# Kernel optimization log

Measured on AMD Instinct MI355X. Metric: run time of the kernel, lower is better.

## Reference

```python
import jax, jax.numpy as jnp
import numpy as np
from jax import lax

EMB, HID, L, PATCH, IMG, K = 192, 64, 6, 4, 224, 8
FMAP = IMG // PATCH
N = FMAP * FMAP
B = 8
ALG = 4
GB_np = np.array([0, 1, 1, 2])  # grade of each blade [1, e1, e2, e12]
GB = jnp.asarray(GB_np)

def _cayley_np():
    C = np.zeros((4, 4, 4), np.float32)
    tbl = {(0,0):(0,1.),(0,1):(1,1.),(0,2):(2,1.),(0,3):(3,1.),
           (1,0):(1,1.),(1,1):(0,1.),(1,2):(3,1.),(1,3):(2,1.),
           (2,0):(2,1.),(2,1):(3,-1.),(2,2):(0,1.),(2,3):(1,-1.),
           (3,0):(3,1.),(3,1):(2,-1.),(3,2):(1,1.),(3,3):(0,-1.)}
    for (i, j), (k, s) in tbl.items():
        C[i, j, k] = s
    return C

CAY_np = _cayley_np()
CAYLEY = jnp.asarray(CAY_np)
_paths = np.zeros((3, 3, 3), bool)
for _i in range(4):
    for _j in range(4):
        for _k in range(4):
            if CAY_np[_i, _j, _k] != 0:
                _paths[GB_np[_i], GB_np[_j], GB_np[_k]] = True
PI, PJ, PK = (jnp.asarray(a) for a in np.nonzero(_paths))
NPATH = int(_paths.sum())  # 10 geometric-product paths for Cl(2,0)

def build_knn_graph(H, W, k):
    yy, xx = np.meshgrid(np.arange(H, dtype=np.float32), np.arange(W, dtype=np.float32), indexing='ij')
    coords = np.stack([xx.ravel(), yy.ravel()], -1)
    cn = coords / np.array([W - 1, H - 1], np.float32) * 2 - 1
    d = np.linalg.norm(cn[:, None] - cn[None], axis=-1)
    np.fill_diagonal(d, np.inf)
    idx = np.argsort(d, axis=-1, kind='stable')[:, :k]
    rows = np.repeat(np.arange(H * W), k)
    cols = idx.reshape(-1)
    return rows.astype(np.int32), cols.astype(np.int32), cn.astype(np.float32)

def mvlin(x, W, b=None):
    # per-grade MVLinear: W [out,in,3] expanded to blades via GB
    y = jnp.einsum('nmi,bmi->bni', W[:, :, GB], x)
    if b is not None:
        y = y.at[:, :, 0].add(b)  # bias embedded in scalar blade only
    return y

def mvlin_flat(x, W, b):
    # subspaces=False MVLinear: same weight across blades
    y = jnp.einsum('nm,bmi->bni', W, x)
    return y.at[:, :, 0].add(b)

def mv_silu(x, a, b):
    # invariants: [scalar, q(grade1), q(grade2)]; gate = sigmoid(a*inv+b)
    inv = jnp.concatenate([x[..., :1], x[..., 1:2]**2 + x[..., 2:3]**2, x[..., 3:4]**2], -1)
    return jax.nn.sigmoid(a * inv + b)[..., GB] * x

def normalize_mv(x, a):
    q = jnp.concatenate([x[..., :1]**2, x[..., 1:2]**2 + x[..., 2:3]**2, x[..., 3:4]**2], -1)
    n = jnp.sqrt(q + 1e-12)
    d = jax.nn.sigmoid(a) * (n - 1.0) + 1.0
    return x / (d + 1e-6)[..., GB]

def sgp(x, Wl, bl, Wr, na, gw):
    # SteerableGeometricProductLayer
    xr = normalize_mv(mvlin(x, Wr), na)
    full = jnp.zeros((gw.shape[0], 3, 3, 3), x.dtype).at[:, PI, PJ, PK].set(gw)
    fb = full[:, GB][:, :, GB][:, :, :, GB]  # [feat,4,4,4]
    gp = jnp.einsum('bni,nijk,bnk->bnj', x, CAYLEY[None] * fb, xr)
    return (mvlin(x, Wl, bl) + gp) * np.float32(1.0 / np.sqrt(2.0))

def _forward(x, conv_w, conv_b, stem_g, stem_b, pos_embed, in_W, in_b, in_Wl, in_bl, in_Wr, in_na, in_gw, eg_eW, eg_eb, eg_sa, eg_sb, eg_nW, eg_nb, eg_Wl, eg_bl, eg_Wr, eg_na, eg_gw, eg_aa, eg_ab, out_W, out_b, on_g, on_b, cls_W, cls_b, coords, rows, cols):
    Bx = x.shape[0]
    # stem: strided conv + LayerNorm over (C,H,W)
    y = lax.conv_general_dilated(x, conv_w, (PATCH, PATCH), 'VALID', dimension_numbers=('NCHW', 'OIHW', 'NCHW')) + conv_b[None, :, None, None]
    mu = y.mean(axis=(1, 2, 3), keepdims=True)
    var = ((y - mu) ** 2).mean(axis=(1, 2, 3), keepdims=True)
    y = (y - mu) / jnp.sqrt(var + 1e-5) * stem_g[None] + stem_b[None]
    y = y + pos_embed
    feat = y.transpose(0, 2, 3, 1).reshape(Bx * N, EMB)
    # embed features in scalar blade, coordinates in vector blades e1,e2
    h = jnp.zeros((Bx * N, EMB + 1, ALG), x.dtype)
    h = h.at[:, :EMB, 0].set(feat)
    h = h.at[:, EMB, 1:3].set(jnp.tile(coords, (Bx, 1)))
    h = sgp(mvlin_flat(h, in_W, in_b), in_Wl, in_bl, in_Wr, in_na, in_gw)
    BN = Bx * N
    for i in range(L):
        m = mv_silu(mvlin(h[rows] - h[cols], eg_eW[i], eg_eb[i]), eg_sa[i], eg_sb[i])
        agg = jax.ops.segment_sum(m, rows, num_segments=BN)  # count computed but unused in original
        nu = mvlin(jnp.concatenate([h, agg], axis=1), eg_nW[i], eg_nb[i])
        out = mv_silu(sgp(nu, eg_Wl[i], eg_bl[i], eg_Wr[i], eg_na[i], eg_gw[i]), eg_aa[i], eg_ab[i])
        h = h + out if i > 0 else out
    s = mvlin_flat(h, out_W, out_b)[..., 0]
    mu2 = s.mean(-1, keepdims=True)
    v2 = ((s - mu2) ** 2).mean(-1, keepdims=True)
    s = (s - mu2) / jnp.sqrt(v2 + 1e-5) * on_g + on_b
    pooled = s.reshape(Bx, N, EMB).mean(axis=1)
    return pooled @ cls_W.T + cls_b

def setup_inputs() -> dict:
    key = jax.random.key(0)
    ks = iter(jax.random.split(key, 64))
    nrm = lambda shape, s=0.05: jax.random.normal(next(ks), shape, jnp.float32) * s
    rows, cols, cn = build_knn_graph(FMAP, FMAP, K)
    offs = np.arange(B, dtype=np.int32)[:, None] * N
    rows_b = (rows[None] + offs).reshape(-1)
    cols_b = (cols[None] + offs).reshape(-1)
    return dict(
        x=jax.random.normal(next(ks), (B, 3, IMG, IMG), jnp.float32),
        conv_w=nrm((EMB, 3, PATCH, PATCH)),
        conv_b=jnp.zeros((EMB,), jnp.float32),
        stem_g=jnp.ones((EMB, FMAP, FMAP), jnp.float32),
        stem_b=jnp.zeros((EMB, FMAP, FMAP), jnp.float32),
        pos_embed=nrm((1, EMB, FMAP, FMAP), 0.02),
        coords=jnp.asarray(cn),
        in_W=nrm((HID, EMB + 1)), in_b=jnp.zeros((HID,), jnp.float32),
        in_Wl=nrm((HID, HID, 3)), in_bl=jnp.zeros((HID,), jnp.float32),
        in_Wr=nrm((HID, HID, 3)), in_na=jnp.zeros((HID, 3), jnp.float32),
        in_gw=nrm((HID, NPATH), 0.2),
        eg_eW=nrm((L, HID, HID, 3)), eg_eb=jnp.zeros((L, HID), jnp.float32),
        eg_sa=jnp.ones((L, HID, 3), jnp.float32), eg_sb=jnp.zeros((L, HID, 3), jnp.float32),
        eg_nW=nrm((L, HID, 2 * HID, 3)), eg_nb=jnp.zeros((L, HID), jnp.float32),
        eg_Wl=nrm((L, HID, HID, 3)), eg_bl=jnp.zeros((L, HID), jnp.float32),
        eg_Wr=nrm((L, HID, HID, 3)), eg_na=jnp.zeros((L, HID, 3), jnp.float32),
        eg_gw=nrm((L, HID, NPATH), 0.2),
        eg_aa=jnp.ones((L, HID, 3), jnp.float32), eg_ab=jnp.zeros((L, HID, 3), jnp.float32),
        out_W=nrm((EMB, HID)), out_b=jnp.zeros((EMB,), jnp.float32),
        on_g=jnp.ones((EMB,), jnp.float32), on_b=jnp.zeros((EMB,), jnp.float32),
        cls_W=nrm((10, EMB), 0.02), cls_b=jnp.zeros((10,), jnp.float32),
        rows=jnp.asarray(rows_b), cols=jnp.asarray(cols_b),
    )

def reference(x, conv_w, conv_b, stem_g, stem_b, pos_embed, coords, in_W, in_b, in_Wl, in_bl, in_Wr, in_na, in_gw, eg_eW, eg_eb, eg_sa, eg_sb, eg_nW, eg_nb, eg_Wl, eg_bl, eg_Wr, eg_na, eg_gw, eg_aa, eg_ab, out_W, out_b, on_g, on_b, cls_W, cls_b, rows, cols):
    return _forward(x, conv_w, conv_b, stem_g, stem_b, pos_embed, in_W, in_b, in_Wl, in_bl, in_Wr, in_na, in_gw, eg_eW, eg_eb, eg_sa, eg_sb, eg_nW, eg_nb, eg_Wl, eg_bl, eg_Wr, eg_na, eg_gw, eg_aa, eg_ab, out_W, out_b, on_g, on_b, cls_W, cls_b, coords, rows, cols)
```

## Files before the change

kernel.cpp:

```cpp
#include <hip/hip_runtime.h>
#include <hip/hip_bf16.h>
#include <math.h>

#define EMBC   192
#define NLAY   6
#define IMGC   224
#define FMAPC  56
#define NNODE  3136
#define NBATCH 8
#define BNODES 25088
#define KNNE   8
#define NT     32
#define RSQRT2 0.70710678118654752f

__device__ __forceinline__ float sigm(float x){ return 1.0f/(1.0f+__expf(-x)); }

__global__ void k_repackw(const float* __restrict__ src, float* __restrict__ dst, int K){
  int l = blockIdx.y;
  size_t S = (size_t)64*K*3;
  int t = blockIdx.x*256 + threadIdx.x;
  if(t < (int)S){
    int j = t % 3; int r = t / 3;
    int cw = r % 16; int m = (r / 16) % K; int widx = r / (16*K);
    dst[l*S + (((size_t)widx*K + m)*16 + cw)*3 + j] =
      src[l*S + ((size_t)(widx*16+cw)*K + m)*3 + j];
  }
}
__global__ void k_repack1(const float* __restrict__ src, float* __restrict__ dst,
                          int R, int K){
  int t = blockIdx.x*256 + threadIdx.x;
  if(t < R*K){
    int m = t % K, r = t / K;
    dst[m*R + r] = src[r*K + m];
  }
}

__global__ void k_tr(const float* __restrict__ g, const float* __restrict__ sb,
                     const float* __restrict__ pe, float* __restrict__ g2,
                     float* __restrict__ pb2){
  int n = blockIdx.x; int c = threadIdx.x;
  g2[n*EMBC + c]  = g[c*NNODE + n];
  pb2[n*EMBC + c] = sb[c*NNODE + n] + pe[c*NNODE + n];
}

__global__ __launch_bounds__(256) void k_conv(const float* __restrict__ x,
    const float* __restrict__ cw, const float* __restrict__ cb,
    float* __restrict__ y0, float* __restrict__ parts){
  __shared__ float xs[2688];
  __shared__ float wsh[9216];
  __shared__ float red[512];
  int blk = blockIdx.x; int b = blk / FMAPC; int ph = blk % FMAPC;
  int tid = threadIdx.x;
  for(int t = tid; t < 9216; t += 256) wsh[t] = cw[t];
  for(int t = tid; t < 2688; t += 256){
    int r = t / IMGC; int w = t % IMGC;
    int ci = r >> 2, kh = r & 3;
    xs[t] = x[((size_t)(b*3 + ci)*IMGC + (ph*4 + kh))*IMGC + w];
  }
  __syncthreads();
  float s1 = 0.f, s2 = 0.f;
  for(int oi = tid; oi < FMAPC*EMBC; oi += 256){
    int pw = oi / EMBC; int c = oi % EMBC;
    float acc = cb[c];
    const float4* wv4 = (const float4*)(wsh + c*48);
    #pragma unroll
    for(int r = 0; r < 12; ++r){
      float4 xv = *((const float4*)(xs + r*IMGC + pw*4));
      float4 wv = wv4[r];
      acc += xv.x*wv.x + xv.y*wv.y + xv.z*wv.z + xv.w*wv.w;
    }
    y0[((size_t)(b*NNODE + ph*FMAPC + pw))*EMBC + c] = acc;
    s1 += acc; s2 += acc*acc;
  }
  red[tid] = s1; red[256+tid] = s2;
  __syncthreads();
  for(int st = 128; st > 0; st >>= 1){
    if(tid < st){ red[tid] += red[tid+st]; red[256+tid] += red[256+tid+st]; }
    __syncthreads();
  }
  if(tid == 0){ parts[blk*2] = red[0]; parts[blk*2+1] = red[256]; }
}

__global__ void k_stats(const float* __restrict__ parts, float* __restrict__ stats){
  int b = threadIdx.x;
  if(b < NBATCH){
    float S = 0.f, Q = 0.f;
    for(int j = 0; j < FMAPC; ++j){ S += parts[(b*FMAPC+j)*2]; Q += parts[(b*FMAPC+j)*2+1]; }
    float cnt = (float)(EMBC*NNODE);
    float mu = S/cnt;
    float var = Q/cnt - mu*mu;
    stats[b*2] = mu; stats[b*2+1] = rsqrtf(var + 1e-5f);
  }
}

__global__ __launch_bounds__(256,2) void k_embed(const float* __restrict__ y0,
    const float* __restrict__ stats, const float* __restrict__ g2,
    const float* __restrict__ pb2, const float* __restrict__ inWp,
    const float* __restrict__ inb, const float* __restrict__ coords,
    float* __restrict__ xmv){
  __shared__ float fs[64*193];
  int tid = threadIdx.x, lane = tid & 63;
  int wid = __builtin_amdgcn_readfirstlane(tid >> 6);
  int ch0 = wid << 4;
  int bid = blockIdx.x;
  int blk = (bid & 7)*49 + (bid >> 3);
  int p0 = blk * 64;
  int b = p0 / NNODE; int n0 = p0 - b*NNODE;
  float mu = stats[b*2], rstd = stats[b*2+1];
  for(int t = tid; t < 64*192; t += 256){
    int n = t / 192, c = t - n*192;
    int nn = n0 + n;
    fs[n*193 + c] = (y0[(size_t)(p0+n)*192 + c] - mu)*rstd*g2[nn*192+c] + pb2[nn*192+c];
  }
  __syncthreads();
  float acc[16];
  #pragma unroll
  for(int ci = 0; ci < 16; ++ci) acc[ci] = 0.f;
  #pragma unroll 2
  for(int m = 0; m < 192; ++m){
    float xm = fs[lane*193 + m];
    const float* wp = inWp + m*64 + ch0;
    #pragma unroll
    for(int ci = 0; ci < 16; ++ci) acc[ci] += wp[ci]*xm;
  }
  float cx = coords[(n0+lane)*2], cy = coords[(n0+lane)*2+1];
  #pragma unroll
  for(int ci = 0; ci < 16; ++ci){
    int ch = ch0 + ci;
    float wc = inWp[192*64 + ch];
    float4 v; v.x = acc[ci] + inb[ch]; v.y = wc*cx; v.z = wc*cy; v.w = 0.f;
    *((float4*)(xmv + ((size_t)(p0+lane)*64 + ch)*4)) = v;
  }
}

__device__ __forceinline__ void stage_x(float* xs, const float* __restrict__ g,
                                        int p0, int tid){
  #pragma unroll
  for(int t = tid; t < NT*64; t += 256){
    int n = t >> 6, m = t & 63;
    *((float4*)(xs + (n<<8) + (((m + n)&63)<<2))) =
      *((const float4*)(g + (((size_t)(p0+n))<<8) + (m<<2)));
  }
}
__device__ __forceinline__ void copyout(const float* xs, float* __restrict__ g,
                                        int p0, int tid){
  #pragma unroll
  for(int t = tid; t < NT*64; t += 256){
    int n = t >> 6, m = t & 63;
    float4 v = *((const float4*)(xs + (n<<8) + (((m + n)&63)<<2)));
    *((float4*)(g + (((size_t)(p0+n))<<8) + (m<<2))) = v;
  }
}
__device__ __forceinline__ void stage_w(float* wst, const float* __restrict__ Wp,
                                        int K, int moff, int tid){
  #pragma unroll
  for(int t = tid; t < 3072; t += 256){
    int c = t / 768, r = t - c*768;
    ((float4*)wst)[t] = ((const float4*)(Wp + ((size_t)(c*K + moff)*48)))[r];
  }
}
__device__ __forceinline__ void mm2n(float (&pA)[4][4], float (&pB)[4][4],
    const float* __restrict__ wst, const float* __restrict__ xrA,
    const float* __restrict__ xrB, int wb, int np){
  #pragma unroll 4
  for(int m = 0; m < 64; ++m){
    float4 xa = *((const float4*)(xrA + (((m + np)&63)<<2)));
    float4 xb = *((const float4*)(xrB + (((m + np + 16)&63)<<2)));
    const float* wp = wst + wb + m*48;
    float4 a = *((const float4*)wp);
    float4 b = *((const float4*)(wp+4));
    float4 c = *((const float4*)(wp+8));
    pA[0][0]+=a.x*xa.x; pA[0][1]+=a.y*xa.y; pA[0][2]+=a.y*xa.z; pA[0][3]+=a.z*xa.w;
    pA[1][0]+=a.w*xa.x; pA[1][1]+=b.x*xa.y; pA[1][2]+=b.x*xa.z; pA[1][3]+=b.y*xa.w;
    pA[2][0]+=b.z*xa.x; pA[2][1]+=b.w*xa.y; pA[2][2]+=b.w*xa.z; pA[2][3]+=c.x*xa.w;
    pA[3][0]+=c.y*xa.x; pA[3][1]+=c.z*xa.y; pA[3][2]+=c.z*xa.z; pA[3][3]+=c.w*xa.w;
    pB[0][0]+=a.x*xb.x; pB[0][1]+=a.y*xb.y; pB[0][2]+=a.y*xb.z; pB[0][3]+=a.z*xb.w;
    pB[1][0]+=a.w*xb.x; pB[1][1]+=b.x*xb.y; pB[1][2]+=b.x*xb.z; pB[1][3]+=b.y*xb.w;
    pB[2][0]+=b.z*xb.x; pB[2][1]+=b.w*xb.y; pB[2][2]+=b.w*xb.z; pB[2][3]+=c.x*xb.w;
    pB[3][0]+=c.y*xb.x; pB[3][1]+=c.z*xb.y; pB[3][2]+=c.z*xb.z; pB[3][3]+=c.w*xb.w;
  }
}
#define ZERO44(A) { _Pragma("unroll") for(int _i=0;_i<4;++_i) _Pragma("unroll") for(int _j=0;_j<4;++_j) A[_i][_j]=0.f; }

__global__ __launch_bounds__(256,2) void k_sgp0(const float* __restrict__ src,
    float* __restrict__ h, float* __restrict__ zout,
    const float* __restrict__ Wlp, const float* __restrict__ bl,
    const float* __restrict__ Wrp, const float* __restrict__ na,
    const float* __restrict__ gw, const float* __restrict__ zWp){
  __shared__ float xs[NT*256];
  __shared__ float wst[12288];
  int tid = threadIdx.x, lane = tid & 63;
  int widx = __builtin_amdgcn_readfirstlane(tid >> 6);
  int np = lane & 15, qw = lane >> 4;
  int ch0 = widx*16 + qw*4;
  int wb = widx*3072 + qw*12;
  int bid = blockIdx.x;
  int blk = (bid & 7)*98 + (bid >> 3);
  int p0 = blk * NT;
  const float* xrA = xs + (np<<8);
  const float* xrB = xs + ((np+16)<<8);
  stage_x(xs, src, p0, tid);
  stage_w(wst, Wlp, 64, 0, tid);
  __syncthreads();
  float lA[4][4], lB[4][4];
  ZERO44(lA); ZERO44(lB);
  mm2n(lA, lB, wst, xrA, xrB, wb, np);
  __syncthreads();
  stage_w(wst, Wrp, 64, 0, tid);
  __syncthreads();
  float rA[4][4], rB[4][4];
  ZERO44(rA); ZERO44(rB);
  mm2n(rA, rB, wst, xrA, xrB, wb, np);
  float oA[4][4], oB[4][4];
  #pragma unroll
  for(int j = 0; j < 2; ++j){
    int nn = np + j*16;
    #pragma unroll
    for(int ci = 0; ci < 4; ++ci){
      int ch = ch0 + ci;
      float yr0 = j? rB[ci][0]:rA[ci][0], yr1 = j? rB[ci][1]:rA[ci][1];
      float yr2 = j? rB[ci][2]:rA[ci][2], yr3 = j? rB[ci][3]:rA[ci][3];
      float na0 = sigm(na[ch*3]), na1 = sigm(na[ch*3+1]), na2 = sigm(na[ch*3+2]);
      float d0 = na0*(sqrtf(yr0*yr0 + 1e-12f) - 1.f) + 1.f + 1e-6f;
      float d1 = na1*(sqrtf(yr1*yr1 + yr2*yr2 + 1e-12f) - 1.f) + 1.f + 1e-6f;
      float d2 = na2*(sqrtf(yr3*yr3 + 1e-12f) - 1.f) + 1.f + 1e-6f;
      float xq0 = yr0/d0, xq1 = yr1/d1, xq2 = yr2/d1, xq3 = yr3/d2;
      float4 xv = *((const float4*)(xs + (nn<<8) + (((ch + nn)&63)<<2)));
      const float* gwp = gw + ch*10;
      float gp0 = gwp[0]*xv.x*xq0 + gwp[3]*(xv.y*xq1 + xv.z*xq2) + gwp[7]*xv.w*xq3;
      float gp1 = gwp[1]*xv.x*xq1 + gwp[4]*xv.y*xq0 - gwp[5]*xv.z*xq3 - gwp[8]*xv.w*xq2;
      float gp2 = gwp[1]*xv.x*xq2 + gwp[4]*xv.z*xq0 + gwp[5]*xv.y*xq3 + gwp[8]*xv.w*xq1;
      float gp3 = gwp[2]*xv.x*xq3 + gwp[6]*(xv.y*xq2 - xv.z*xq1) - gwp[9]*xv.w*xq0;
      float l0 = j? lB[ci][0]:lA[ci][0], l1 = j? lB[ci][1]:lA[ci][1];
      float l2 = j? lB[ci][2]:lA[ci][2], l3 = j? lB[ci][3]:lA[ci][3];
      float* o = j? oB[ci] : oA[ci];
      o[0] = (l0 + bl[ch] + gp0)*RSQRT2;
      o[1] = (l1 + gp1)*RSQRT2;
      o[2] = (l2 + gp2)*RSQRT2;
      o[3] = (l3 + gp3)*RSQRT2;
    }
  }
  __syncthreads();
  #pragma unroll
  for(int ci = 0; ci < 4; ++ci){
    int ch = ch0 + ci;
    float4 v0; v0.x=oA[ci][0]; v0.y=oA[ci][1]; v0.z=oA[ci][2]; v0.w=oA[ci][3];
    *((float4*)(xs + (np<<8) + (((ch + np)&63)<<2))) = v0;
    float4 v1; v1.x=oB[ci][0]; v1.y=oB[ci][1]; v1.z=oB[ci][2]; v1.w=oB[ci][3];
    *((float4*)(xs + ((np+16)<<8) + (((ch + np + 16)&63)<<2))) = v1;
  }
  __syncthreads();
  copyout(xs, h, p0, tid);
  stage_w(wst, zWp, 64, 0, tid);
  __syncthreads();
  float zA[4][4], zB[4][4];
  ZERO44(zA); ZERO44(zB);
  mm2n(zA, zB, wst, xrA, xrB, wb, np);
  __syncthreads();
  #pragma unroll
  for(int ci = 0; ci < 4; ++ci){
    int ch = ch0 + ci;
    float4 v0; v0.x=zA[ci][0]; v0.y=zA[ci][1]; v0.z=zA[ci][2]; v0.w=zA[ci][3];
    *((float4*)(xs + (np<<8) + (((ch + np)&63)<<2))) = v0;
    float4 v1; v1.x=zB[ci][0]; v1.y=zB[ci][1]; v1.z=zB[ci][2]; v1.w=zB[ci][3];
    *((float4*)(xs + ((np+16)<<8) + (((ch + np + 16)&63)<<2))) = v1;
  }
  __syncthreads();
  copyout(xs, zout, p0, tid);
}

__global__ __launch_bounds__(256,2) void k_layer(
    float* __restrict__ h, const float* __restrict__ z,
    float* __restrict__ zout, const int* __restrict__ cols,
    const float* __restrict__ eb, const float* __restrict__ sa,
    const float* __restrict__ sb,
    const float* __restrict__ nWp, const float* __restrict__ nb,
    const float* __restrict__ Wlp, const float* __restrict__ bl,
    const float* __restrict__ Wrp, const float* __restrict__ na,
    const float* __restrict__ gw, const float* __restrict__ aa,
    const float* __restrict__ ab,
    const float* __restrict__ zWp, int mode){
  __shared__ float xs[NT*256];
  __shared__ float wst[12288];
  int tid = threadIdx.x, lane = tid & 63;
  int widx = __builtin_amdgcn_readfirstlane(tid >> 6);
  int np = lane & 15, qw = lane >> 4;
  int ch0 = widx*16 + qw*4;
  int wb = widx*3072 + qw*12;
  int bid = blockIdx.x;
  int blk = (bid & 7)*98 + (bid >> 3);
  int p0 = blk * NT;
  const float* xrA = xs + (np<<8);
  const float* xrB = xs + ((np+16)<<8);
  float ag[8][4];
  {
    int ch = lane;
    float ebv = eb[ch];
    float a0 = sa[ch*3], a1 = sa[ch*3+1], a2 = sa[ch*3+2];
    float b0 = sb[ch*3], b1 = sb[ch*3+1], b2 = sb[ch*3+2];
    #pragma unroll
    for(int e = 0; e < 8; ++e){
      int p = p0 + widx*8 + e;
      float4 zo = *((const float4*)(z + ((size_t)p*64 + ch)*4));
      float ax=0.f, ay=0.f, az_=0.f, aw=0.f;
      #pragma unroll
      for(int k = 0; k < KNNE; ++k){
        int c = cols[p*KNNE + k];
        float4 zc = *((const float4*)(z + ((size_t)c*64 + ch)*4));
        float d0 = zo.x - zc.x + ebv;
        float d1 = zo.y - zc.y;
        float d2 = zo.z - zc.z;
        float d3 = zo.w - zc.w;
        float g0 = sigm(a0*d0 + b0);
        float g1 = sigm(a1*(d1*d1 + d2*d2) + b1);
        float g2v = sigm(a2*(d3*d3) + b2);
        ax += g0*d0; ay += g1*d1; az_ += g1*d2; aw += g2v*d3;
      }
      ag[e][0]=ax; ag[e][1]=ay; ag[e][2]=az_; ag[e][3]=aw;
    }
  }
  stage_x(xs, h, p0, tid);
  stage_w(wst, nWp, 128, 0, tid);
  __syncthreads();
  float nuA[4][4], nuB[4][4];
  ZERO44(nuA); ZERO44(nuB);
  mm2n(nuA, nuB, wst, xrA, xrB, wb, np);
  float hrA[4][4], hrB[4][4];
  if(mode == 2){
    #pragma unroll
    for(int ci = 0; ci < 4; ++ci){
      int ch = ch0 + ci;
      float4 v0 = *((const float4*)(xrA + (((ch + np)&63)<<2)));
      float4 v1 = *((const float4*)(xrB + (((ch + np + 16)&63)<<2)));
      hrA[ci][0]=v0.x; hrA[ci][1]=v0.y; hrA[ci][2]=v0.z; hrA[ci][3]=v0.w;
      hrB[ci][0]=v1.x; hrB[ci][1]=v1.y; hrB[ci][2]=v1.z; hrB[ci][3]=v1.w;
    }
  }
  __syncthreads();
  #pragma unroll
  for(int e = 0; e < 8; ++e){
    int nn = widx*8 + e;
    float4 v; v.x=ag[e][0]; v.y=ag[e][1]; v.z=ag[e][2]; v.w=ag[e][3];
    *((float4*)(xs + (nn<<8) + (((lane + nn)&63)<<2))) = v;
  }
  stage_w(wst, nWp, 128, 64, tid);
  __syncthreads();
  mm2n(nuA, nuB, wst, xrA, xrB, wb, np);
  __syncthreads();
  #pragma unroll
  for(int ci = 0; ci < 4; ++ci){
    int ch = ch0 + ci;
    nuA[ci][0] += nb[ch]; nuB[ci][0] += nb[ch];
    float4 v0; v0.x=nuA[ci][0]; v0.y=nuA[ci][1]; v0.z=nuA[ci][2]; v0.w=nuA[ci][3];
    *((float4*)(xs + (np<<8) + (((ch + np)&63)<<2))) = v0;
    float4 v1; v1.x=nuB[ci][0]; v1.y=nuB[ci][1]; v1.z=nuB[ci][2]; v1.w=nuB[ci][3];
    *((float4*)(xs + ((np+16)<<8) + (((ch + np + 16)&63)<<2))) = v1;
  }
  stage_w(wst, Wlp, 64, 0, tid);
  __syncthreads();
  float lA[4][4], lB[4][4];
  ZERO44(lA); ZERO44(lB);
  mm2n(lA, lB, wst, xrA, xrB, wb, np);
  __syncthreads();
  stage_w(wst, Wrp, 64, 0, tid);
  __syncthreads();
  float rA[4][4], rB[4][4];
  ZERO44(rA); ZERO44(rB);
  mm2n(rA, rB, wst, xrA, xrB, wb, np);
  float oA[4][4], oB[4][4];
  #pragma unroll
  for(int j = 0; j < 2; ++j){
    #pragma unroll
    for(int ci = 0; ci < 4; ++ci){
      int ch = ch0 + ci;
      float yr0 = j? rB[ci][0]:rA[ci][0], yr1 = j? rB[ci][1]:rA[ci][1];
      float yr2 = j? rB[ci][2]:rA[ci][2], yr3 = j? rB[ci][3]:rA[ci][3];
      float na0 = sigm(na[ch*3]), na1 = sigm(na[ch*3+1]), na2 = sigm(na[ch*3+2]);
      float d0 = na0*(sqrtf(yr0*yr0 + 1e-12f) - 1.f) + 1.f + 1e-6f;
      float d1 = na1*(sqrtf(yr1*yr1 + yr2*yr2 + 1e-12f) - 1.f) + 1.f + 1e-6f;
      float d2 = na2*(sqrtf(yr3*yr3 + 1e-12f) - 1.f) + 1.f + 1e-6f;
      float xq0 = yr0/d0, xq1 = yr1/d1, xq2 = yr2/d1, xq3 = yr3/d2;
      float x0 = j? nuB[ci][0]:nuA[ci][0], x1 = j? nuB[ci][1]:nuA[ci][1];
      float x2 = j? nuB[ci][2]:nuA[ci][2], x3 = j? nuB[ci][3]:nuA[ci][3];
      const float* gwp = gw + ch*10;
      float gp0 = gwp[0]*x0*xq0 + gwp[3]*(x1*xq1 + x2*xq2) + gwp[7]*x3*xq3;
      float gp1 = gwp[1]*x0*xq1 + gwp[4]*x1*xq0 - gwp[5]*x2*xq3 - gwp[8]*x3*xq2;
      float gp2 = gwp[1]*x0*xq2 + gwp[4]*x2*xq0 + gwp[5]*x1*xq3 + gwp[8]*x3*xq1;
      float gp3 = gwp[2]*x0*xq3 + gwp[6]*(x1*xq2 - x2*xq1) - gwp[9]*x3*xq0;
      float l0 = j? lB[ci][0]:lA[ci][0], l1 = j? lB[ci][1]:lA[ci][1];
      float l2 = j? lB[ci][2]:lA[ci][2], l3 = j? lB[ci][3]:lA[ci][3];
      float o0 = (l0 + bl[ch] + gp0)*RSQRT2;
      float o1 = (l1 + gp1)*RSQRT2;
      float o2 = (l2 + gp2)*RSQRT2;
      float o3 = (l3 + gp3)*RSQRT2;
      float g0 = sigm(aa[ch*3]*o0 + ab[ch*3]);
      float g1 = sigm(aa[ch*3+1]*(o1*o1 + o2*o2) + ab[ch*3+1]);
      float g2v = sigm(aa[ch*3+2]*(o3*o3) + ab[ch*3+2]);
      float v0 = g0*o0, v1 = g1*o1, v2 = g1*o2, v3 = g2v*o3;
      if(mode == 2){
        if(j){ v0 += hrB[ci][0]; v1 += hrB[ci][1]; v2 += hrB[ci][2]; v3 += hrB[ci][3]; }
        else { v0 += hrA[ci][0]; v1 += hrA[ci][1]; v2 += hrA[ci][2]; v3 += hrA[ci][3]; }
      }
      float* o = j? oB[ci] : oA[ci];
      o[0]=v0; o[1]=v1; o[2]=v2; o[3]=v3;
    }
  }
  __syncthreads();
  #pragma unroll
  for(int ci = 0; ci < 4; ++ci){
    int ch = ch0 + ci;
    float4 v0; v0.x=oA[ci][0]; v0.y=oA[ci][1]; v0.z=oA[ci][2]; v0.w=oA[ci][3];
    *((float4*)(xs + (np<<8) + (((ch + np)&63)<<2))) = v0;
    float4 v1; v1.x=oB[ci][0]; v1.y=oB[ci][1]; v1.z=oB[ci][2]; v1.w=oB[ci][3];
    *((float4*)(xs + ((np+16)<<8) + (((ch + np + 16)&63)<<2))) = v1;
  }
  __syncthreads();
  copyout(xs, h, p0, tid);
  if(zWp != nullptr){
    stage_w(wst, zWp, 64, 0, tid);
    __syncthreads();
    float zA[4][4], zB[4][4];
    ZERO44(zA); ZERO44(zB);
    mm2n(zA, zB, wst, xrA, xrB, wb, np);
    __syncthreads();
    #pragma unroll
    for(int ci = 0; ci < 4; ++ci){
      int ch = ch0 + ci;
      float4 v0; v0.x=zA[ci][0]; v0.y=zA[ci][1]; v0.z=zA[ci][2]; v0.w=zA[ci][3];
      *((float4*)(xs + (np<<8) + (((ch + np)&63)<<2))) = v0;
      float4 v1; v1.x=zB[ci][0]; v1.y=zB[ci][1]; v1.z=zB[ci][2]; v1.w=zB[ci][3];
      *((float4*)(xs + ((np+16)<<8) + (((ch + np + 16)&63)<<2))) = v1;
    }
    __syncthreads();
    copyout(xs, zout, p0, tid);
  }
}

__global__ __launch_bounds__(256,2) void k_head(const float* __restrict__ h,
    const float* __restrict__ oWp, const float* __restrict__ ob,
    const float* __restrict__ ong, const float* __restrict__ onb,
    float* __restrict__ s){
  __shared__ float hs[64*65];
  __shared__ float rr[512];
  int tid = threadIdx.x, lane = tid & 63;
  int wid = __builtin_amdgcn_readfirstlane(tid >> 6);
  int c0 = wid*48;
  int bid = blockIdx.x;
  int blk = (bid & 7)*49 + (bid >> 3);
  int p0 = blk * 64;
  for(int t = tid; t < 64*64; t += 256){
    int nn = t >> 6, c = t & 63;
    hs[nn*65 + c] = h[(((size_t)(p0+nn))*64 + c)*4];
  }
  __syncthreads();
  float a[48];
  #pragma unroll
  for(int ci = 0; ci < 48; ++ci) a[ci] = 0.f;
  #pragma unroll 2
  for(int m = 0; m < 64; ++m){
    float xm = hs[lane*65 + m];
    const float* wp = oWp + m*192 + c0;
    #pragma unroll
    for(int ci = 0; ci < 48; ++ci) a[ci] += wp[ci]*xm;
  }
  float s1 = 0.f, s2 = 0.f;
  #pragma unroll
  for(int ci = 0; ci < 48; ++ci){
    a[ci] += ob[c0+ci];
    s1 += a[ci]; s2 += a[ci]*a[ci];
  }
  rr[wid*64 + lane] = s1; rr[256 + wid*64 + lane] = s2;
  __syncthreads();
  float S = rr[lane] + rr[64+lane] + rr[128+lane] + rr[192+lane];
  float Q = rr[256+lane] + rr[320+lane] + rr[384+lane] + rr[448+lane];
  float mu = S*(1.0f/EMBC);
  float var = Q*(1.0f/EMBC) - mu*mu;
  float rstd = rsqrtf(var + 1e-5f);
  #pragma unroll
  for(int q = 0; q < 12; ++q){
    int c = c0 + q*4;
    float4 v;
    v.x = (a[q*4  ] - mu)*rstd*ong[c  ] + onb[c  ];
    v.y = (a[q*4+1] - mu)*rstd*ong[c+1] + onb[c+1];
    v.z = (a[q*4+2] - mu)*rstd*ong[c+2] + onb[c+2];
    v.w = (a[q*4+3] - mu)*rstd*ong[c+3] + onb[c+3];
    *((float4*)(s + (size_t)(p0+lane)*192 + c)) = v;
  }
}

__global__ void k_pool1(const float* __restrict__ s, float* __restrict__ pp){
  int blk = blockIdx.x;
  int b = blk >> 5, chunk = blk & 31;
  int c = threadIdx.x;
  float acc = 0.f;
  int n0 = chunk*98;
  for(int j = 0; j < 98; ++j) acc += s[((size_t)(b*NNODE + n0 + j))*EMBC + c];
  pp[(size_t)blk*EMBC + c] = acc;
}
__global__ void k_pool2(const float* __restrict__ pp, float* __restrict__ pooled){
  int b = blockIdx.x; int c = threadIdx.x;
  float acc = 0.f;
  for(int j = 0; j < 32; ++j) acc += pp[((size_t)(b*32 + j))*EMBC + c];
  pooled[b*EMBC + c] = acc * (1.0f/NNODE);
}

__global__ void k_cls(const float* __restrict__ pooled, const float* __restrict__ cW,
                      const float* __restrict__ cb, float* __restrict__ out){
  int tid = threadIdx.x;
  if(tid < NBATCH*10){
    int b = tid/10, k = tid%10;
    float acc = cb[k];
    for(int c = 0; c < EMBC; ++c) acc += pooled[b*EMBC + c]*cW[k*EMBC + c];
    out[tid] = acc;
  }
}

extern "C" void kernel_launch(void* const* d_in, const int* in_sizes, int n_in,
                              void* d_out, int out_size, void* d_ws, size_t ws_size,
                              hipStream_t stream){
  const float* x      = (const float*)d_in[0];
  const float* conv_w = (const float*)d_in[1];
  const float* conv_b = (const float*)d_in[2];
  const float* stem_g = (const float*)d_in[3];
  const float* stem_b = (const float*)d_in[4];
  const float* pos_e  = (const float*)d_in[5];
  const float* coords = (const float*)d_in[6];
  const float* inW    = (const float*)d_in[7];
  const float* inb    = (const float*)d_in[8];
  const float* inWl   = (const float*)d_in[9];
  const float* inbl   = (const float*)d_in[10];
  const float* inWr   = (const float*)d_in[11];
  const float* inna   = (const float*)d_in[12];
  const float* ingw   = (const float*)d_in[13];
  const float* eg_eW  = (const float*)d_in[14];
  const float* eg_eb  = (const float*)d_in[15];
  const float* eg_sa  = (const float*)d_in[16];
  const float* eg_sb  = (const float*)d_in[17];
  const float* eg_nW  = (const float*)d_in[18];
  const float* eg_nb  = (const float*)d_in[19];
  const float* eg_Wl  = (const float*)d_in[20];
  const float* eg_bl  = (const float*)d_in[21];
  const float* eg_Wr  = (const float*)d_in[22];
  const float* eg_na  = (const float*)d_in[23];
  const float* eg_gw  = (const float*)d_in[24];
  const float* eg_aa  = (const float*)d_in[25];
  const float* eg_ab  = (const float*)d_in[26];
  const float* outW   = (const float*)d_in[27];
  const float* outb   = (const float*)d_in[28];
  const float* ong    = (const float*)d_in[29];
  const float* onb    = (const float*)d_in[30];
  const float* clsW   = (const float*)d_in[31];
  const float* clsb   = (const float*)d_in[32];
  const int*   cols   = (const int*)d_in[34];

  float* ws = (float*)d_ws;
  size_t off = 0;
  float* hbuf  = ws + off; off += (size_t)BNODES*256;
  float* bigA  = ws + off; off += (size_t)BNODES*256;
  float* bigB  = ws + off; off += (size_t)BNODES*256;
  float* g2    = ws + off; off += (size_t)NNODE*EMBC;
  float* pb2   = ws + off; off += (size_t)NNODE*EMBC;
  float* parts = ws + off; off += 896;
  float* stats = ws + off; off += 16;
  float* pp    = ws + off; off += 256*EMBC;
  float* pooled= ws + off; off += NBATCH*EMBC;
  float* wpInW = ws + off; off += 193*64;
  float* wpOW  = ws + off; off += 64*192;
  float* wpInWl= ws + off; off += 12288;
  float* wpInWr= ws + off; off += 12288;
  float* wpEW  = ws + off; off += (size_t)NLAY*12288;
  float* wpWl  = ws + off; off += (size_t)NLAY*12288;
  float* wpWr  = ws + off; off += (size_t)NLAY*12288;
  float* wpNW  = ws + off; off += (size_t)NLAY*24576;
  float* y0    = bigB;

  const int NTILE = BNODES/NT;

  { dim3 g1((12352+255)/256); k_repack1<<<g1, 256, 0, stream>>>(inW,  wpInW, 64, 193); }
  { dim3 g1((12288+255)/256); k_repack1<<<g1, 256, 0, stream>>>(outW, wpOW, 192, 64); }
  { dim3 g3((12288+255)/256, 1); k_repackw<<<g3, 256, 0, stream>>>(inWl, wpInWl, 64); }
  { dim3 g3((12288+255)/256, 1); k_repackw<<<g3, 256, 0, stream>>>(inWr, wpInWr, 64); }
  { dim3 g3((12288+255)/256, NLAY); k_repackw<<<g3, 256, 0, stream>>>(eg_eW, wpEW, 64); }
  { dim3 g3((12288+255)/256, NLAY); k_repackw<<<g3, 256, 0, stream>>>(eg_Wl, wpWl, 64); }
  { dim3 g3((12288+255)/256, NLAY); k_repackw<<<g3, 256, 0, stream>>>(eg_Wr, wpWr, 64); }
  { dim3 g3((24576+255)/256, NLAY); k_repackw<<<g3, 256, 0, stream>>>(eg_nW, wpNW, 128); }

  k_tr   <<<NNODE, 192, 0, stream>>>(stem_g, stem_b, pos_e, g2, pb2);
  k_conv <<<NBATCH*FMAPC, 256, 0, stream>>>(x, conv_w, conv_b, y0, parts);
  k_stats<<<1, 64, 0, stream>>>(parts, stats);
  k_embed<<<BNODES/64, 256, 0, stream>>>(y0, stats, g2, pb2, wpInW, inb, coords, bigA);
  k_sgp0 <<<NTILE, 256, 0, stream>>>(bigA, hbuf, bigB, wpInWl, inbl, wpInWr,
                                     inna, ingw, wpEW);
  float* zcur = bigB;
  float* spare = bigA;
  for(int l = 0; l < NLAY; ++l){
    const float* zWn = (l < NLAY-1) ? (wpEW + (size_t)(l+1)*12288) : (const float*)nullptr;
    k_layer<<<NTILE, 256, 0, stream>>>(hbuf, zcur, spare, cols,
        eg_eb + l*64, eg_sa + l*192, eg_sb + l*192,
        wpNW + (size_t)l*24576, eg_nb + l*64,
        wpWl + (size_t)l*12288, eg_bl + l*64,
        wpWr + (size_t)l*12288, eg_na + l*192,
        eg_gw + l*640, eg_aa + l*192, eg_ab + l*192,
        zWn, (l==0)?1:2);
    if(l < NLAY-1){ float* t = zcur; zcur = spare; spare = t; }
  }
  k_head <<<BNODES/64, 256, 0, stream>>>(hbuf, wpOW, outb, ong, onb, spare);
  k_pool1<<<256, 192, 0, stream>>>(spare, pp);
  k_pool2<<<8, 192, 0, stream>>>(pp, pooled);
  k_cls  <<<1, 128, 0, stream>>>(pooled, clsW, clsb, (float*)d_out);
}
```

Baseline: 1.493 ms.

## Stream weights in 16-row chunks to shrink LDS and raise occupancy

Weight staging is split into four 16-input-channel chunks per matmul, each staged between barriers, so the LDS weight buffer shrinks from 48KB to 12KB. Launch bounds rise from 2 to 3 blocks per CU to use the freed LDS for more resident workgroups. The cost is four times as many barriers and smaller, unoverlapped global-to-LDS loads per pass, plus tighter register limits that may cause spilling.

```diff
diff --git a/kernel.cpp b/kernel.cpp
--- a/kernel.cpp
+++ b/kernel.cpp
@@ -151,21 +151,22 @@
     *((float4*)(g + (((size_t)(p0+n))<<8) + (m<<2))) = v;
   }
 }
-__device__ __forceinline__ void stage_w(float* wst, const float* __restrict__ Wp,
-                                        int K, int moff, int tid){
-  #pragma unroll
-  for(int t = tid; t < 3072; t += 256){
-    int c = t / 768, r = t - c*768;
+__device__ __forceinline__ void stage_w16(float* wst, const float* __restrict__ Wp,
+                                          int K, int moff, int tid){
+  #pragma unroll
+  for(int t = tid; t < 768; t += 256){
+    int c = t / 192, r = t - c*192;
     ((float4*)wst)[t] = ((const float4*)(Wp + ((size_t)(c*K + moff)*48)))[r];
   }
 }
-__device__ __forceinline__ void mm2n(float (&pA)[4][4], float (&pB)[4][4],
+__device__ __forceinline__ void mm2n16(float (&pA)[4][4], float (&pB)[4][4],
     const float* __restrict__ wst, const float* __restrict__ xrA,
-    const float* __restrict__ xrB, int wb, int np){
+    const float* __restrict__ xrB, int wb, int np, int mo){
   #pragma unroll 4
-  for(int m = 0; m < 64; ++m){
-    float4 xa = *((const float4*)(xrA + (((m + np)&63)<<2)));
-    float4 xb = *((const float4*)(xrB + (((m + np + 16)&63)<<2)));
+  for(int m = 0; m < 16; ++m){
+    int mg = mo + m;
+    float4 xa = *((const float4*)(xrA + (((mg + np)&63)<<2)));
+    float4 xb = *((const float4*)(xrB + (((mg + np + 16)&63)<<2)));
     const float* wp = wst + wb + m*48;
     float4 a = *((const float4*)wp);
     float4 b = *((const float4*)(wp+4));
@@ -180,37 +181,44 @@
     pB[3][0]+=c.y*xb.x; pB[3][1]+=c.z*xb.y; pB[3][2]+=c.z*xb.z; pB[3][3]+=c.w*xb.w;
   }
 }
+__device__ __forceinline__ void mmpass(float (&pA)[4][4], float (&pB)[4][4],
+    float* wst, const float* __restrict__ Wp, int K, int mbase,
+    const float* __restrict__ xrA, const float* __restrict__ xrB,
+    int wb, int np, int tid){
+  #pragma unroll
+  for(int mo = 0; mo < 64; mo += 16){
+    __syncthreads();
+    stage_w16(wst, Wp, K, mbase + mo, tid);
+    __syncthreads();
+    mm2n16(pA, pB, wst, xrA, xrB, wb, np, mo);
+  }
+}
 #define ZERO44(A) { _Pragma("unroll") for(int _i=0;_i<4;++_i) _Pragma("unroll") for(int _j=0;_j<4;++_j) A[_i][_j]=0.f; }
 
-__global__ __launch_bounds__(256,2) void k_sgp0(const float* __restrict__ src,
+__global__ __launch_bounds__(256,3) void k_sgp0(const float* __restrict__ src,
     float* __restrict__ h, float* __restrict__ zout,
     const float* __restrict__ Wlp, const float* __restrict__ bl,
     const float* __restrict__ Wrp, const float* __restrict__ na,
     const float* __restrict__ gw, const float* __restrict__ zWp){
   __shared__ float xs[NT*256];
-  __shared__ float wst[12288];
+  __shared__ float wst[3072];
   int tid = threadIdx.x, lane = tid & 63;
   int widx = __builtin_amdgcn_readfirstlane(tid >> 6);
   int np = lane & 15, qw = lane >> 4;
   int ch0 = widx*16 + qw*4;
-  int wb = widx*3072 + qw*12;
+  int wb = widx*768 + qw*12;
   int bid = blockIdx.x;
   int blk = (bid & 7)*98 + (bid >> 3);
   int p0 = blk * NT;
   const float* xrA = xs + (np<<8);
   const float* xrB = xs + ((np+16)<<8);
   stage_x(xs, src, p0, tid);
-  stage_w(wst, Wlp, 64, 0, tid);
-  __syncthreads();
   float lA[4][4], lB[4][4];
   ZERO44(lA); ZERO44(lB);
-  mm2n(lA, lB, wst, xrA, xrB, wb, np);
-  __syncthreads();
-  stage_w(wst, Wrp, 64, 0, tid);
-  __syncthreads();
+  mmpass(lA, lB, wst, Wlp, 64, 0, xrA, xrB, wb, np, tid);
   float rA[4][4], rB[4][4];
   ZERO44(rA); ZERO44(rB);
-  mm2n(rA, rB, wst, xrA, xrB, wb, np);
+  mmpass(rA, rB, wst, Wrp, 64, 0, xrA, xrB, wb, np, tid);
   float oA[4][4], oB[4][4];
   #pragma unroll
   for(int j = 0; j < 2; ++j){
@@ -251,11 +259,9 @@
   }
   __syncthreads();
   copyout(xs, h, p0, tid);
-  stage_w(wst, zWp, 64, 0, tid);
-  __syncthreads();
   float zA[4][4], zB[4][4];
   ZERO44(zA); ZERO44(zB);
-  mm2n(zA, zB, wst, xrA, xrB, wb, np);
+  mmpass(zA, zB, wst, zWp, 64, 0, xrA, xrB, wb, np, tid);
   __syncthreads();
   #pragma unroll
   for(int ci = 0; ci < 4; ++ci){
@@ -269,7 +275,7 @@
   copyout(xs, zout, p0, tid);
 }
 
-__global__ __launch_bounds__(256,2) void k_layer(
+__global__ __launch_bounds__(256,3) void k_layer(
     float* __restrict__ h, const float* __restrict__ z,
     float* __restrict__ zout, const int* __restrict__ cols,
     const float* __restrict__ eb, const float* __restrict__ sa,
@@ -281,12 +287,12 @@
     const float* __restrict__ ab,
     const float* __restrict__ zWp, int mode){
   __shared__ float xs[NT*256];
-  __shared__ float wst[12288];
+  __shared__ float wst[3072];
   int tid = threadIdx.x, lane = tid & 63;
   int widx = __builtin_amdgcn_readfirstlane(tid >> 6);
   int np = lane & 15, qw = lane >> 4;
   int ch0 = widx*16 + qw*4;
-  int wb = widx*3072 + qw*12;
+  int wb = widx*768 + qw*12;
   int bid = blockIdx.x;
   int blk = (bid & 7)*98 + (bid >> 3);
   int p0 = blk * NT;
@@ -320,11 +326,9 @@
     }
   }
   stage_x(xs, h, p0, tid);
-  stage_w(wst, nWp, 128, 0, tid);
-  __syncthreads();
   float nuA[4][4], nuB[4][4];
   ZERO44(nuA); ZERO44(nuB);
-  mm2n(nuA, nuB, wst, xrA, xrB, wb, np);
+  mmpass(nuA, nuB, wst, nWp, 128, 0, xrA, xrB, wb, np, tid);
   float hrA[4][4], hrB[4][4];
   if(mode == 2){
     #pragma unroll
@@ -343,9 +347,7 @@
     float4 v; v.x=ag[e][0]; v.y=ag[e][1]; v.z=ag[e][2]; v.w=ag[e][3];
     *((float4*)(xs + (nn<<8) + (((lane + nn)&63)<<2))) = v;
   }
-  stage_w(wst, nWp, 128, 64, tid);
-  __syncthreads();
-  mm2n(nuA, nuB, wst, xrA, xrB, wb, np);
+  mmpass(nuA, nuB, wst, nWp, 128, 64, xrA, xrB, wb, np, tid);
   __syncthreads();
   #pragma unroll
   for(int ci = 0; ci < 4; ++ci){
@@ -356,17 +358,12 @@
     float4 v1; v1.x=nuB[ci][0]; v1.y=nuB[ci][1]; v1.z=nuB[ci][2]; v1.w=nuB[ci][3];
     *((float4*)(xs + ((np+16)<<8) + (((ch + np + 16)&63)<<2))) = v1;
   }
-  stage_w(wst, Wlp, 64, 0, tid);
-  __syncthreads();
   float lA[4][4], lB[4][4];
   ZERO44(lA); ZERO44(lB);
-  mm2n(lA, lB, wst, xrA, xrB, wb, np);
-  __syncthreads();
-  stage_w(wst, Wrp, 64, 0, tid);
-  __syncthreads();
+  mmpass(lA, lB, wst, Wlp, 64, 0, xrA, xrB, wb, np, tid);
   float rA[4][4], rB[4][4];
   ZERO44(rA); ZERO44(rB);
-  mm2n(rA, rB, wst, xrA, xrB, wb, np);
+  mmpass(rA, rB, wst, Wrp, 64, 0, xrA, xrB, wb, np, tid);
   float oA[4][4], oB[4][4];
   #pragma unroll
   for(int j = 0; j < 2; ++j){
@@ -417,11 +414,9 @@
   __syncthreads();
   copyout(xs, h, p0, tid);
   if(zWp != nullptr){
-    stage_w(wst, zWp, 64, 0, tid);
-    __syncthreads();
     float zA[4][4], zB[4][4];
     ZERO44(zA); ZERO44(zB);
-    mm2n(zA, zB, wst, xrA, xrB, wb, np);
+    mmpass(zA, zB, wst, zWp, 64, 0, xrA, xrB, wb, np, tid);
     __syncthreads();
     #pragma unroll
     for(int ci = 0; ci < 4; ++ci){
```

Result: slower. 2.166 ms (+45.1%).
